# Optimization experiments

Hardware: AMD Instinct MI355X
Metric: run time of the kernel (lower is better)

## Reference

```python
import jax, jax.numpy as jnp
import numpy as np

EPS = 1e-8


def setup_inputs() -> dict:
    key = jax.random.key(0)
    k1, k2, k3 = jax.random.split(key, 3)
    B, N, K, D = 64, 4096, 64, 256
    x = jax.random.normal(k1, (B, N, D), dtype=jnp.float32)
    mu = jax.random.normal(k2, (K, D), dtype=jnp.float32)
    log_sigma = jax.random.normal(k3, (K, D), dtype=jnp.float32) * 0.1
    return {"x": x, "mu": mu, "log_sigma": log_sigma, "n_slots": 8}


def reference(x, mu, log_sigma, n_slots):
    # cosine similarity: normalize then contract (avoids [B,N,K,D] broadcast)
    xn = x / jnp.maximum(jnp.linalg.norm(x, axis=-1, keepdims=True), EPS)
    mn = mu / jnp.maximum(jnp.linalg.norm(mu, axis=-1, keepdims=True), EPS)
    cos = jnp.einsum('bnd,kd->bnk', xn, mn)            # [B, N, K]
    cos_soft = jax.nn.softmax(cos, axis=-1)            # softmax over concepts
    r = jax.nn.softmax(cos_soft.sum(axis=1), axis=-1)  # [B, K]
    _, idx = jax.lax.top_k(r, n_slots)                 # [B, n_slots]
    mu_sample = mu[idx]                                # [B, n_slots, D]
    sigma_sample = jnp.exp(log_sigma[idx])             # [B, n_slots, D]
    noise = jax.random.normal(jax.random.key(42), mu_sample.shape, dtype=mu_sample.dtype)
    return mu_sample + sigma_sample * noise
```

## Files before the change

kernel.cpp:

```cpp
#include <hip/hip_runtime.h>
#include <math.h>
#include <stdint.h>

#define B_ 64
#define N_ 4096
#define K_ 64
#define D_ 256
#define NS_ 8

__device__ __forceinline__ float fadd(float a, float b) { return __fadd_rn(a, b); }
__device__ __forceinline__ float fmul(float a, float b) { return __fmul_rn(a, b); }

__device__ __forceinline__ float np_expf(float x) {
  const float LOG2E = 1.442695040888963407359924681001892137f;
  float qf = rintf(__fmul_rn(x, LOG2E));
  float r = __fmaf_rn(qf, -6.93145752e-1f, x);
  r = __fmaf_rn(qf, -1.42860677e-6f, r);
  float num = __fmaf_rn(r, 5.082762527590693718096e-04f, 6.757896990527504603057e-03f);
  num = __fmaf_rn(num, r, 5.114512081637298353406e-02f);
  num = __fmaf_rn(num, r, 2.473615434895520810817e-01f);
  num = __fmaf_rn(num, r, 7.257664613233124478488e-01f);
  num = __fmaf_rn(num, r, 9.999999999980870924916e-01f);
  float den = __fmaf_rn(r, 2.159509375685829852307e-02f, -2.742335390411667452936e-01f);
  den = __fmaf_rn(den, r, 1.000000000000000000000e+00f);
  float poly = __fdiv_rn(num, den);
  int qi = (int)qf;
  float scale = __int_as_float((127 + qi) << 23);
  return __fmul_rn(poly, scale);
}

__device__ __forceinline__ uint32_t rotl32(uint32_t x, int r) {
  return (x << r) | (x >> (32 - r));
}
__device__ __forceinline__ float jax_normal_from_index(uint32_t i) {
  uint32_t x0 = 0u, x1 = i;
  const uint32_t ks0 = 0u, ks1 = 42u, ks2 = 0x1BD11BDAu ^ 0u ^ 42u;
  x0 += ks0; x1 += ks1;
#define TF_ROUND(r) { x0 += x1; x1 = rotl32(x1, (r)); x1 ^= x0; }
  TF_ROUND(13) TF_ROUND(15) TF_ROUND(26) TF_ROUND(6)
  x0 += ks1; x1 += ks2 + 1u;
  TF_ROUND(17) TF_ROUND(29) TF_ROUND(16) TF_ROUND(24)
  x0 += ks2; x1 += ks0 + 2u;
  TF_ROUND(13) TF_ROUND(15) TF_ROUND(26) TF_ROUND(6)
  x0 += ks0; x1 += ks1 + 3u;
  TF_ROUND(17) TF_ROUND(29) TF_ROUND(16) TF_ROUND(24)
  x0 += ks1; x1 += ks2 + 4u;
  TF_ROUND(13) TF_ROUND(15) TF_ROUND(26) TF_ROUND(6)
  x0 += ks2; x1 += ks0 + 5u;
#undef TF_ROUND
  uint32_t bits = x0 ^ x1;
  uint32_t fb = (bits >> 9) | 0x3f800000u;
  float f = __uint_as_float(fb) - 1.0f;
  const float lo = __uint_as_float(0xBF7FFFFFu);
  float u = f * 2.0f + lo;
  u = fmaxf(lo, u);
  float w = -log1pf(-u * u);
  float p;
  if (w < 5.0f) {
    w = w - 2.5f;
    p = 2.81022636e-08f;
    p = fmaf(p, w, 3.43273939e-07f);
    p = fmaf(p, w, -3.5233877e-06f);
    p = fmaf(p, w, -4.39150654e-06f);
    p = fmaf(p, w, 0.00021858087f);
    p = fmaf(p, w, -0.00125372503f);
    p = fmaf(p, w, -0.00417768164f);
    p = fmaf(p, w, 0.246640727f);
    p = fmaf(p, w, 1.50140941f);
  } else {
    w = sqrtf(w) - 3.0f;
    p = -0.000200214257f;
    p = fmaf(p, w, 0.000100950558f);
    p = fmaf(p, w, 0.00134934322f);
    p = fmaf(p, w, -0.00367342844f);
    p = fmaf(p, w, 0.00573950773f);
    p = fmaf(p, w, -0.0076224613f);
    p = fmaf(p, w, 0.00943887047f);
    p = fmaf(p, w, 1.00167406f);
    p = fmaf(p, w, 2.83297682f);
  }
  return 1.41421356f * (p * u);
}

__device__ __forceinline__ float np_pw128_sq(const float* p) {
  float t16[16];
#pragma unroll
  for (int L = 0; L < 16; ++L) {
    float q0 = p[L];       q0 = fmul(q0, q0);
    float q1 = p[L + 16];  q1 = fmul(q1, q1);
    float q2 = p[L + 32];  q2 = fmul(q2, q2);
    float q3 = p[L + 48];  q3 = fmul(q3, q3);
    float q4 = p[L + 64];  q4 = fmul(q4, q4);
    float q5 = p[L + 80];  q5 = fmul(q5, q5);
    float q6 = p[L + 96];  q6 = fmul(q6, q6);
    float q7 = p[L + 112]; q7 = fmul(q7, q7);
    t16[L] = fadd(fadd(fadd(q0, q4), fadd(q1, q5)), fadd(fadd(q2, q6), fadd(q3, q7)));
  }
  float u8[8];
#pragma unroll
  for (int L = 0; L < 8; ++L) u8[L] = fadd(t16[L], t16[L + 8]);
  float v4[4];
#pragma unroll
  for (int L = 0; L < 4; ++L) v4[L] = fadd(u8[L], u8[L + 4]);
  return fadd(fadd(v4[0], v4[2]), fadd(v4[1], v4[3]));
}

__device__ __forceinline__ float np_sum64(const float* a) {
  float t16[16];
#pragma unroll
  for (int L = 0; L < 16; ++L)
    t16[L] = fadd(fadd(a[L], a[16 + L]), fadd(a[32 + L], a[48 + L]));
  float u8[8];
#pragma unroll
  for (int L = 0; L < 8; ++L) u8[L] = fadd(t16[L], t16[L + 8]);
  float v4[4];
#pragma unroll
  for (int L = 0; L < 4; ++L) v4[L] = fadd(u8[L], u8[L + 4]);
  return fadd(fadd(v4[0], v4[2]), fadd(v4[1], v4[3]));
}

__global__ __launch_bounds__(64)
void prep_mnT(const float* __restrict__ mu, float4* __restrict__ mnT4) {
  const int k = threadIdx.x;
  const float* mrow = mu + k * D_;
  const float n2 = fadd(np_pw128_sq(mrow), np_pw128_sq(mrow + 128));
  const float den = fmaxf(__fsqrt_rn(n2), 1e-8f);
#pragma unroll 8
  for (int t = 0; t < 64; ++t) {
    float4 m = *(const float4*)&mrow[4 * t];
    float4 o;
    o.x = __fdiv_rn(m.x, den); o.y = __fdiv_rn(m.y, den);
    o.z = __fdiv_rn(m.z, den); o.w = __fdiv_rn(m.w, den);
    mnT4[t * K_ + k] = o;
  }
}

__global__ __launch_bounds__(1024, 1)
void xn_cos_softmax(const float* __restrict__ x,
                    const float4* __restrict__ mnT4_g,
                    float* __restrict__ p_ws) {
  __shared__ float4 mnT4[64][64];
  __shared__ float xst[16][4][256];

  const int b = blockIdx.x;
  const int seg = blockIdx.y;
  const int tid = threadIdx.x;
  const int w = tid >> 6;
  const int lane = tid & 63;

#pragma unroll
  for (int i = 0; i < 4; ++i)
    ((float4*)mnT4)[tid * 4 + i] = mnT4_g[tid * 4 + i];
  __syncthreads();

  const int L16 = lane & 15;
  const int rowg = lane >> 4;

  for (int pass = 0; pass < 8; ++pass) {
    const int n0 = seg * 512 + pass * 64 + w * 4;

#pragma unroll
    for (int r = 0; r < 4; ++r) {
      const float4 v = *(const float4*)&x[(((size_t)b << 12) + n0 + r) * D_ + lane * 4];
      *(float4*)&xst[w][r][lane * 4] = v;
    }
    __syncthreads();

    float den4[4];
    {
      const float* rowp = &xst[w][rowg][0];
      float res2[2];
#pragma unroll
      for (int half = 0; half < 2; ++half) {
        const float* p = rowp + half * 128 + L16;
        float q0 = p[0];   q0 = fmul(q0, q0);
        float q1 = p[16];  q1 = fmul(q1, q1);
        float q2 = p[32];  q2 = fmul(q2, q2);
        float q3 = p[48];  q3 = fmul(q3, q3);
        float q4 = p[64];  q4 = fmul(q4, q4);
        float q5 = p[80];  q5 = fmul(q5, q5);
        float q6 = p[96];  q6 = fmul(q6, q6);
        float q7 = p[112]; q7 = fmul(q7, q7);
        const float t = fadd(fadd(fadd(q0, q4), fadd(q1, q5)),
                             fadd(fadd(q2, q6), fadd(q3, q7)));
        float u  = fadd(t, __shfl_xor(t, 8));
        float v  = fadd(u, __shfl_xor(u, 4));
        float w2 = fadd(v, __shfl_xor(v, 2));
        res2[half] = fadd(w2, __shfl_xor(w2, 1));
      }
      const float n2 = fadd(res2[0], res2[1]);
      const float den = fmaxf(__fsqrt_rn(n2), 1e-8f);
#pragma unroll
      for (int r = 0; r < 4; ++r) den4[r] = __shfl(den, 16 * r);
    }
    __syncthreads();

#pragma unroll
    for (int r = 0; r < 4; ++r) {
      float4 v = *(float4*)&xst[w][r][lane * 4];
      v.x = __fdiv_rn(v.x, den4[r]); v.y = __fdiv_rn(v.y, den4[r]);
      v.z = __fdiv_rn(v.z, den4[r]); v.w = __fdiv_rn(v.w, den4[r]);
      *(float4*)&xst[w][r][lane * 4] = v;
    }
    __syncthreads();

    float acc[4][4];
#pragma unroll
    for (int r = 0; r < 4; ++r)
#pragma unroll
      for (int j = 0; j < 4; ++j) acc[r][j] = 0.f;

#pragma unroll 4
    for (int t = 0; t < 64; ++t) {
      const float4 m4 = mnT4[t][lane];
#pragma unroll
      for (int r = 0; r < 4; ++r) {
        const float4 x4 = *(const float4*)&xst[w][r][4 * t];
        acc[r][0] = fadd(acc[r][0], fmul(x4.x, m4.x));
        acc[r][1] = fadd(acc[r][1], fmul(x4.y, m4.y));
        acc[r][2] = fadd(acc[r][2], fmul(x4.z, m4.z));
        acc[r][3] = fadd(acc[r][3], fmul(x4.w, m4.w));
      }
    }

#pragma unroll
    for (int r = 0; r < 4; ++r) {
      const float cosr = fadd(fadd(acc[r][0], acc[r][1]), fadd(acc[r][2], acc[r][3]));
      float mx = cosr;
      mx = fmaxf(mx, __shfl_xor(mx, 1));
      mx = fmaxf(mx, __shfl_xor(mx, 2));
      mx = fmaxf(mx, __shfl_xor(mx, 4));
      mx = fmaxf(mx, __shfl_xor(mx, 8));
      mx = fmaxf(mx, __shfl_xor(mx, 16));
      mx = fmaxf(mx, __shfl_xor(mx, 32));
      const float e = np_expf(__fsub_rn(cosr, mx));
      float g1 = fadd(e, __shfl_xor(e, 16));
      float g2 = fadd(g1, __shfl_xor(g1, 32));
      float u  = fadd(g2, __shfl_xor(g2, 8));
      float v  = fadd(u, __shfl_xor(u, 4));
      float w2 = fadd(v, __shfl_xor(v, 2));
      float sres = fadd(w2, __shfl_xor(w2, 1));
      const float denom = __shfl(sres, 0);
      const float p = __fdiv_rn(e, denom);
      p_ws[(((size_t)b << 12) + n0 + r) * K_ + lane] = p;
    }
    __syncthreads();
  }
}

__global__ __launch_bounds__(256)
void pairwise_sum_n(const float* __restrict__ p_ws, float* __restrict__ s_part) {
  __shared__ float part[4][K_];
  const int b = blockIdx.x;
  const int g = blockIdx.y;
  const int w = threadIdx.x >> 6;
  const int k = threadIdx.x & 63;
  const float* base = p_ws + ((size_t)b << 12) * K_ + k;

  float l[2];
#pragma unroll 1
  for (int i = 0; i < 2; ++i) {
    const float* leaf = base + (size_t)(g * 8 + w * 2 + i) * 128 * K_;
    float c[16];
#pragma unroll
    for (int L = 0; L < 16; ++L) {
      const float* pL = leaf + (size_t)L * K_;
      const float q0 = pL[0 * 16 * K_];
      const float q1 = pL[1 * 16 * K_];
      const float q2 = pL[2 * 16 * K_];
      const float q3 = pL[3 * 16 * K_];
      const float q4 = pL[4 * 16 * K_];
      const float q5 = pL[5 * 16 * K_];
      const float q6 = pL[6 * 16 * K_];
      const float q7 = pL[7 * 16 * K_];
      c[L] = fadd(fadd(fadd(q0, q4), fadd(q1, q5)), fadd(fadd(q2, q6), fadd(q3, q7)));
    }
    float u8[8];
#pragma unroll
    for (int L = 0; L < 8; ++L) u8[L] = fadd(c[L], c[L + 8]);
    float v4[4];
#pragma unroll
    for (int L = 0; L < 4; ++L) v4[L] = fadd(u8[L], u8[L + 4]);
    l[i] = fadd(fadd(v4[0], v4[2]), fadd(v4[1], v4[3]));
  }
  part[w][k] = fadd(l[0], l[1]);
  __syncthreads();
  if (w == 0) {
    const float Sg = fadd(fadd(part[0][k], part[1][k]), fadd(part[2][k], part[3][k]));
    s_part[(b * 4 + g) * K_ + k] = Sg;
  }
}

__global__ __launch_bounds__(256)
void topk_sample(const float* __restrict__ s_part,
                 const float* __restrict__ mu,
                 const float* __restrict__ ls,
                 float* __restrict__ out) {
  __shared__ float sv[K_];
  __shared__ int sidx[NS_];
  const int b = blockIdx.x;
  const int t = threadIdx.x;
  if (t < K_) {
    const float S0 = s_part[(b * 4 + 0) * K_ + t];
    const float S1 = s_part[(b * 4 + 1) * K_ + t];
    const float S2 = s_part[(b * 4 + 2) * K_ + t];
    const float S3 = s_part[(b * 4 + 3) * K_ + t];
    sv[t] = fadd(fadd(S0, S1), fadd(S2, S3));
  }
  __syncthreads();
  if (t == 0) {
    float mx = sv[0];
    for (int k = 1; k < K_; ++k) mx = fmaxf(mx, sv[k]);
    float e[K_];
    for (int k = 0; k < K_; ++k) e[k] = np_expf(__fsub_rn(sv[k], mx));
    const float denom = np_sum64(e);
    float rv[K_];
    for (int k = 0; k < K_; ++k) rv[k] = __fdiv_rn(e[k], denom);
    for (int q = 0; q < NS_; ++q) {
      float best = -1.0e30f; int bi = 0;
      for (int k = 0; k < K_; ++k) {
        if (rv[k] > best) { best = rv[k]; bi = k; }
      }
      sidx[q] = bi;
      rv[bi] = -1.0e30f;
    }
  }
  __syncthreads();

  const int q = t >> 5;
  const int d0 = (t & 31) * 8;
  const int k = sidx[q];
  const float* mrow = mu + k * D_ + d0;
  const float* lrow = ls + k * D_ + d0;
  float* orow = out + ((size_t)b * NS_ + q) * D_ + d0;
  const uint32_t ibase = (uint32_t)(((b * NS_) + q) * D_ + d0);
#pragma unroll
  for (int j = 0; j < 8; ++j) {
    const float z = jax_normal_from_index(ibase + (uint32_t)j);
    orow[j] = fmaf(expf(lrow[j]), z, mrow[j]);
  }
}

extern "C" void kernel_launch(void* const* d_in, const int* in_sizes, int n_in,
                              void* d_out, int out_size, void* d_ws, size_t ws_size,
                              hipStream_t stream) {
  const float* x  = (const float*)d_in[0];
  const float* mu = (const float*)d_in[1];
  const float* ls = (const float*)d_in[2];
  float* out = (float*)d_out;
  (void)ws_size; (void)in_sizes; (void)n_in; (void)out_size;

  float*  p_ws   = (float*)d_ws;
  float*  s_part = (float*)((char*)d_ws + (size_t)67108864);
  float4* mnT4   = (float4*)((char*)d_ws + (size_t)67174400);

  prep_mnT<<<1, 64, 0, stream>>>(mu, mnT4);
  dim3 grid(B_, 8);
  xn_cos_softmax<<<grid, 1024, 0, stream>>>(x, mnT4, p_ws);
  dim3 grid2(B_, 4);
  pairwise_sum_n<<<grid2, 256, 0, stream>>>(p_ws, s_part);
  topk_sample<<<B_, 256, 0, stream>>>(s_part, mu, ls, out);
}
```

Baseline: 325.1 us.

## Prefetch next x tile into registers and replace block barriers with wave-local fences

Loads the next pass's x rows into registers while the current pass computes, so global-load latency overlaps the norm, matmul and softmax work. Since each wave only touches its own xst slice, the block-wide __syncthreads are swapped for lgkmcnt waits and compiler barriers. It also pads the xst rows to avoid LDS bank conflicts. This depends on wave-private LDS access staying correct without block barriers, and it costs extra registers for the prefetch buffer.

```diff
diff --git a/kernel.cpp b/kernel.cpp
--- a/kernel.cpp
+++ b/kernel.cpp
@@ -7,6 +7,10 @@
 #define K_ 64
 #define D_ 256
 #define NS_ 8
+#define XPAD 260
+
+#define FENCE_LGKM() asm volatile("s_waitcnt lgkmcnt(0)" ::: "memory")
+#define CBAR() asm volatile("" ::: "memory")
 
 __device__ __forceinline__ float fadd(float a, float b) { return __fadd_rn(a, b); }
 __device__ __forceinline__ float fmul(float a, float b) { return __fmul_rn(a, b); }
@@ -140,7 +144,7 @@
                     const float4* __restrict__ mnT4_g,
                     float* __restrict__ p_ws) {
   __shared__ float4 mnT4[64][64];
-  __shared__ float xst[16][4][256];
+  __shared__ float xst[16][4][XPAD];
 
   const int b = blockIdx.x;
   const int seg = blockIdx.y;
@@ -156,15 +160,28 @@
   const int L16 = lane & 15;
   const int rowg = lane >> 4;
 
+  float4 xr[4];
+  {
+    const int n0 = seg * 512 + w * 4;
+#pragma unroll
+    for (int r = 0; r < 4; ++r)
+      xr[r] = *(const float4*)&x[(((size_t)b << 12) + n0 + r) * D_ + lane * 4];
+  }
+
   for (int pass = 0; pass < 8; ++pass) {
     const int n0 = seg * 512 + pass * 64 + w * 4;
 
 #pragma unroll
-    for (int r = 0; r < 4; ++r) {
-      const float4 v = *(const float4*)&x[(((size_t)b << 12) + n0 + r) * D_ + lane * 4];
-      *(float4*)&xst[w][r][lane * 4] = v;
-    }
-    __syncthreads();
+    for (int r = 0; r < 4; ++r)
+      *(float4*)&xst[w][r][lane * 4] = xr[r];
+    FENCE_LGKM();
+
+    if (pass < 7) {
+      const int n1 = n0 + 64;
+#pragma unroll
+      for (int r = 0; r < 4; ++r)
+        xr[r] = *(const float4*)&x[(((size_t)b << 12) + n1 + r) * D_ + lane * 4];
+    }
 
     float den4[4];
     {
@@ -193,7 +210,7 @@
 #pragma unroll
       for (int r = 0; r < 4; ++r) den4[r] = __shfl(den, 16 * r);
     }
-    __syncthreads();
+    CBAR();
 
 #pragma unroll
     for (int r = 0; r < 4; ++r) {
@@ -202,7 +219,7 @@
       v.z = __fdiv_rn(v.z, den4[r]); v.w = __fdiv_rn(v.w, den4[r]);
       *(float4*)&xst[w][r][lane * 4] = v;
     }
-    __syncthreads();
+    FENCE_LGKM();
 
     float acc[4][4];
 #pragma unroll
@@ -244,7 +261,7 @@
       const float p = __fdiv_rn(e, denom);
       p_ws[(((size_t)b << 12) + n0 + r) * K_ + lane] = p;
     }
-    __syncthreads();
+    CBAR();
   }
 }
 
```

Result: faster. 312.4 us (-3.9%).
